# Optimization experiments

Hardware: AMD Instinct MI355X
Metric: run time of the kernel (lower is better)

The kernel has to match this reference:

```python
import jax, jax.numpy as jnp
import numpy as np

B, L, D, H, DFF = 4, 2048, 1024, 16, 4096
DH = D // H  # head dim = 64
EPS = 1e-5


def layernorm(x, g, b):
    mu = jnp.mean(x, axis=-1, keepdims=True)
    var = jnp.mean(jnp.square(x - mu), axis=-1, keepdims=True)
    return (x - mu) * jax.lax.rsqrt(var + EPS) * g + b


def setup_inputs() -> dict:
    key = jax.random.key(0)
    ks = jax.random.split(key, 16)
    s = 0.02
    return {
        "X": jax.random.normal(ks[0], (B, L, D), jnp.float32),
        "WQ": jax.random.normal(ks[1], (D, D), jnp.float32) * s,
        "bQ": jnp.zeros((D,), jnp.float32),
        "WK": jax.random.normal(ks[2], (D, D), jnp.float32) * s,
        "bK": jnp.zeros((D,), jnp.float32),
        "WV": jax.random.normal(ks[3], (D, D), jnp.float32) * s,
        "bV": jnp.zeros((D,), jnp.float32),
        "WO": jax.random.normal(ks[4], (D, D), jnp.float32) * s,
        "bO": jnp.zeros((D,), jnp.float32),
        "W1": jax.random.normal(ks[5], (D, DFF), jnp.float32) * s,
        "b1": jnp.zeros((DFF,), jnp.float32),
        "W2": jax.random.normal(ks[6], (DFF, D), jnp.float32) * s,
        "b2": jnp.zeros((D,), jnp.float32),
        "g1": jnp.ones((D,), jnp.float32),
        "be1": jnp.zeros((D,), jnp.float32),
        "g2": jnp.ones((D,), jnp.float32),
        "be2": jnp.zeros((D,), jnp.float32),
    }


def reference(X, WQ, bQ, WK, bK, WV, bV, WO, bO, W1, b1, W2, b2, g1, be1, g2, be2):
    # --- causal self-attention on LayerNorm1(X) ---
    Xn = layernorm(X, g1, be1)
    def heads(W, b):
        return (Xn @ W + b).reshape(B, L, H, DH).transpose(0, 2, 1, 3)  # [B,H,L,DH]
    Q, K, V = heads(WQ, bQ), heads(WK, bK), heads(WV, bV)
    scale = 1.0 / jnp.sqrt(jnp.float32(DH))
    scores = jnp.einsum('bhld,bhsd->bhls', Q, K) * scale  # [B,H,L,L]
    causal = jnp.tril(jnp.ones((L, L), dtype=bool))
    scores = jnp.where(causal, scores, -jnp.inf)
    attn = jax.nn.softmax(scores, axis=-1)
    AV = jnp.einsum('bhls,bhsd->bhld', attn, V)  # [B,H,L,DH]
    AV = AV.transpose(0, 2, 1, 3).reshape(B, L, H * DH)
    X = X + AV @ WO + bO
    # --- MLP on LayerNorm2(X) ---
    Xn2 = layernorm(X, g2, be2)
    out = X + jax.nn.relu(Xn2 @ W1 + b1) @ W2 + b2
    return out
```

## Files before the change

### kernel.cpp

```cpp
#include <hip/hip_runtime.h>
#include <hip/hip_bf16.h>
#include <stdint.h>

#define B_   4
#define L_   2048
#define D_   1024
#define H_   16
#define DH_  64
#define DFF_ 4096
#define EPS_ 1e-5f

typedef short s16x8 __attribute__((ext_vector_type(8)));
typedef short s16x4 __attribute__((ext_vector_type(4)));
typedef float f32x4 __attribute__((ext_vector_type(4)));

static __device__ __forceinline__ short f2bf(float f) {
    return __builtin_bit_cast(short, __float2bfloat16(f));
}

static __device__ __forceinline__ short f2bf_fast(float f) {
    return (short)((__builtin_bit_cast(unsigned int, f) + 0x8000u) >> 16);
}

static __device__ __forceinline__ void gload_lds16(const void* g, void* l) {
    __builtin_amdgcn_global_load_lds(
        (const __attribute__((address_space(1))) uint32_t*)g,
        (__attribute__((address_space(3))) uint32_t*)l, 16, 0, 0);
}

__global__ __launch_bounds__(256) void transpose_kernel(
    const float* __restrict__ in, short* __restrict__ out, int R, int C)
{
    __shared__ float tile[32][33];
    const int bx = blockIdx.x * 32, by = blockIdx.y * 32;
    const int tx = threadIdx.x & 31, ty = threadIdx.x >> 5;
#pragma unroll
    for (int i = 0; i < 32; i += 8)
        tile[ty + i][tx] = in[(size_t)(by + ty + i) * C + bx + tx];
    __syncthreads();
#pragma unroll
    for (int i = 0; i < 32; i += 8)
        out[(size_t)(bx + ty + i) * R + by + tx] = f2bf(tile[tx][ty + i]);
}

__global__ __launch_bounds__(256) void concat3_kernel(
    const float* __restrict__ a, const float* __restrict__ b,
    const float* __restrict__ c, float* __restrict__ o)
{
    const int i = blockIdx.x * 256 + threadIdx.x;
    o[i] = (i < 1024) ? a[i] : (i < 2048 ? b[i - 1024] : c[i - 2048]);
}

__global__ __launch_bounds__(256) void vtrans_kernel(
    const short* __restrict__ V, short* __restrict__ Vt)
{
    __shared__ short t[64][72];
    const int l0 = blockIdx.x * 64;
    const int bh = blockIdx.y;
    const int b = bh >> 4, h = bh & 15;
    const int tid = threadIdx.x;
    const int rr = tid >> 3, cc = tid & 7;
#pragma unroll
    for (int i = 0; i < 2; ++i) {
        const int row = i * 32 + rr;
        *(s16x8*)&t[row][cc * 8] =
            *(const s16x8*)(V + (size_t)(b * L_ + l0 + row) * D_ + h * DH_ + cc * 8);
    }
    __syncthreads();
#pragma unroll
    for (int i = 0; i < 2; ++i) {
        const int d = i * 32 + rr;
        const int lp0 = cc * 8;
        s16x8 o;
#pragma unroll
        for (int j = 0; j < 8; ++j) o[j] = t[lp0 + j][d];
        *(s16x8*)(Vt + ((size_t)bh * DH_ + d) * L_ + l0 + lp0) = o;
    }
}

__global__ __launch_bounds__(256) void ln_kernel(
    const float* __restrict__ x, const float* __restrict__ g,
    const float* __restrict__ bta, short* __restrict__ out)
{
    __shared__ float sm[8];
    const int row = blockIdx.x;
    const int t = threadIdx.x;
    const float4 v = ((const float4*)(x + (size_t)row * D_))[t];
    float s1 = v.x + v.y + v.z + v.w;
    float s2 = v.x * v.x + v.y * v.y + v.z * v.z + v.w * v.w;
#pragma unroll
    for (int off = 1; off < 64; off <<= 1) {
        s1 += __shfl_xor(s1, off);
        s2 += __shfl_xor(s2, off);
    }
    if ((t & 63) == 0) { sm[t >> 6] = s1; sm[4 + (t >> 6)] = s2; }
    __syncthreads();
    s1 = sm[0] + sm[1] + sm[2] + sm[3];
    s2 = sm[4] + sm[5] + sm[6] + sm[7];
    const float mu  = s1 * (1.f / D_);
    const float var = s2 * (1.f / D_) - mu * mu;
    const float rs  = rsqrtf(var + EPS_);
    const float4 gv = ((const float4*)g)[t];
    const float4 bv = ((const float4*)bta)[t];
    s16x4 o;
    o[0] = f2bf((v.x - mu) * rs * gv.x + bv.x);
    o[1] = f2bf((v.y - mu) * rs * gv.y + bv.y);
    o[2] = f2bf((v.z - mu) * rs * gv.z + bv.z);
    o[3] = f2bf((v.w - mu) * rs * gv.w + bv.w);
    *(s16x4*)(out + (size_t)row * D_ + t * 4) = o;
}

template <int MODE>
__global__ __launch_bounds__(512) void gemm_kernel(
    const short* __restrict__ A, const short* __restrict__ Bt,
    const float* __restrict__ bias, const float* __restrict__ res,
    void* __restrict__ out, int M, int N, int K)
{
    __shared__ short As[3][128 * 64];
    __shared__ short Bs[3][256 * 64];

    const int nx = gridDim.x;
    const int flat = blockIdx.y * nx + blockIdx.x;
    const int nper = (nx * gridDim.y) >> 3;
    const int nid = (flat & 7) * nper + (flat >> 3);
    const int m0 = (nid / nx) * 128;
    const int n0 = (nid % nx) * 256;

    const int tid = threadIdx.x;
    const int w = tid >> 6, l = tid & 63;
    const int wm = w >> 2, wn = w & 3;
    const int lg = l >> 4, li = l & 15;

    const short* aSrc[2];
    int adst[2];
#pragma unroll
    for (int i = 0; i < 2; ++i) {
        const int s = i * 512 + tid;
        const int row = s >> 3;
        const int ch = (s & 7) ^ (row & 7);
        aSrc[i] = A + (size_t)(m0 + row) * K + ch * 8;
        adst[i] = s * 8;
    }
    const short* bSrc[4];
    int bdst[4];
#pragma unroll
    for (int i = 0; i < 4; ++i) {
        const int s = i * 512 + tid;
        const int row = s >> 3;
        const int ch = (s & 7) ^ (row & 7);
        bSrc[i] = Bt + (size_t)(n0 + row) * K + ch * 8;
        bdst[i] = s * 8;
    }

    int aoff[4][2], boff[4][2];
#pragma unroll
    for (int m = 0; m < 4; ++m)
#pragma unroll
        for (int ks = 0; ks < 2; ++ks) {
            const int rowA = wm * 64 + m * 16 + li;
            aoff[m][ks] = rowA * 64 + (((ks * 4 + lg) ^ (rowA & 7)) * 8);
        }
#pragma unroll
    for (int n = 0; n < 4; ++n)
#pragma unroll
        for (int ks = 0; ks < 2; ++ks) {
            const int rowB = wn * 64 + n * 16 + li;
            boff[n][ks] = rowB * 64 + (((ks * 4 + lg) ^ (rowB & 7)) * 8);
        }

    f32x4 acc[4][4] = {};
    const int nT = K >> 6;

#pragma unroll
    for (int i = 0; i < 2; ++i) gload_lds16(aSrc[i], &As[0][adst[i]]);
#pragma unroll
    for (int i = 0; i < 4; ++i) gload_lds16(bSrc[i], &Bs[0][bdst[i]]);

    int cur = 0, nxt = 1;
    for (int t = 0; t < nT; ++t) {
        if (t + 1 < nT) {
            const int k1 = (t + 1) << 6;
#pragma unroll
            for (int i = 0; i < 2; ++i) gload_lds16(aSrc[i] + k1, &As[nxt][adst[i]]);
#pragma unroll
            for (int i = 0; i < 4; ++i) gload_lds16(bSrc[i] + k1, &Bs[nxt][bdst[i]]);
            asm volatile("s_waitcnt vmcnt(6)" ::: "memory");
        } else {
            asm volatile("s_waitcnt vmcnt(0)" ::: "memory");
        }
        __builtin_amdgcn_s_barrier();
        __builtin_amdgcn_sched_barrier(0);

        const short* as = &As[cur][0];
        const short* bs = &Bs[cur][0];
        s16x8 af[4][2], bf[4][2];
#pragma unroll
        for (int m = 0; m < 4; ++m)
#pragma unroll
            for (int ks = 0; ks < 2; ++ks)
                af[m][ks] = *(const s16x8*)&as[aoff[m][ks]];
#pragma unroll
        for (int n = 0; n < 4; ++n)
#pragma unroll
            for (int ks = 0; ks < 2; ++ks)
                bf[n][ks] = *(const s16x8*)&bs[boff[n][ks]];
#pragma unroll
        for (int ks = 0; ks < 2; ++ks)
#pragma unroll
            for (int m = 0; m < 4; ++m)
#pragma unroll
                for (int n = 0; n < 4; ++n)
                    acc[m][n] = __builtin_amdgcn_mfma_f32_16x16x32_bf16(
                        af[m][ks], bf[n][ks], acc[m][n], 0, 0, 0);

        cur = nxt;
        nxt = (nxt == 2) ? 0 : nxt + 1;
    }

#pragma unroll
    for (int m = 0; m < 4; ++m) {
#pragma unroll
        for (int n = 0; n < 4; ++n) {
            const int col = n0 + wn * 64 + n * 16 + li;
            const float bv = bias[col];
#pragma unroll
            for (int r = 0; r < 4; ++r) {
                const int row = m0 + wm * 64 + m * 16 + lg * 4 + r;
                float v = acc[m][n][r] + bv;
                if (MODE == 1) v = v > 0.f ? v : 0.f;
                if (MODE == 2) {
                    float* o = (float*)out;
                    o[(size_t)row * N + col] = v + res[(size_t)row * N + col];
                } else if (MODE == 3) {
                    short* o = (short*)out;
                    o[(size_t)(col >> 10) * (8192ull * 1024) +
                      (size_t)row * 1024 + (col & 1023)] = f2bf(v);
                } else {
                    short* o = (short*)out;
                    o[(size_t)row * N + col] = f2bf(v);
                }
            }
        }
    }
}

__global__ __launch_bounds__(512) void attn_kernel(
    const short* __restrict__ Q, const short* __restrict__ K,
    const short* __restrict__ Vt, short* __restrict__ O)
{
    __shared__ short Kbuf[3][64 * 64];
    __shared__ short Vbuf[3][64 * 64];
    __shared__ short Ps[8][16 * 72];

    const int xx = blockIdx.x;
    const int h = blockIdx.y, b = blockIdx.z;
    const int pr = xx >> 1;
    const int u = (pr + b * 2) & 7;
    const int qblk = ((xx + b) & 1) ? (15 - u) : u;
    const int tid = threadIdx.x;
    const int w = tid >> 6, l = tid & 63;
    const int lg = l >> 4, li = l & 15;
    const size_t headQ = ((size_t)b * L_) * D_ + (size_t)h * DH_;
    const size_t headV = ((size_t)(b * H_ + h) * DH_) * L_;
    const int q0 = qblk * 128;
    const int qw = q0 + w * 16;
    const float sc2 = 0.125f * 1.44269504f;

    s16x8 qf[2];
    {
        const short* qr = Q + headQ + (size_t)(qw + li) * D_;
        qf[0] = *(const s16x8*)(qr + lg * 8);
        qf[1] = *(const s16x8*)(qr + 32 + lg * 8);
    }

    const int srow = tid >> 3;
    const int schk = (tid & 7) ^ (srow & 7);
    const short* kSrc = K + headQ + (size_t)srow * D_ + schk * 8;
    const short* vSrc = Vt + headV + (size_t)srow * L_ + schk * 8;

    int koff0[4], koff1[4];
#pragma unroll
    for (int blk = 0; blk < 4; ++blk) {
        const int row = blk * 16 + li;
        const int hh = row & 7;
        koff0[blk] = row * 64 + ((lg ^ hh) * 8);
        koff1[blk] = row * 64 + (((lg + 4) ^ hh) * 8);
    }

    float m_r = -1e30f, l_r = 0.f;
    f32x4 oacc[4] = {};
    short* pw = &Ps[w][0];

    const int nt = 2 * qblk + 2;

    gload_lds16(kSrc, &Kbuf[0][tid * 8]);
    gload_lds16(vSrc, &Vbuf[0][tid * 8]);

    int cur = 0, nxt = 1;
    for (int t = 0; t < nt; ++t) {
        const int kv0 = t * 64;
        if (t + 1 < nt) {
            const int nkv = kv0 + 64;
            gload_lds16(kSrc + (size_t)nkv * D_, &Kbuf[nxt][tid * 8]);
            gload_lds16(vSrc + nkv, &Vbuf[nxt][tid * 8]);
            asm volatile("s_waitcnt vmcnt(2)" ::: "memory");
        } else {
            asm volatile("s_waitcnt vmcnt(0)" ::: "memory");
        }
        __builtin_amdgcn_s_barrier();
        __builtin_amdgcn_sched_barrier(0);

        if (kv0 <= qw + 15) {
            const short* kb = &Kbuf[cur][0];
            const short* vb = &Vbuf[cur][0];

            f32x4 s[4];
            __builtin_amdgcn_s_setprio(1);
#pragma unroll
            for (int blk = 0; blk < 4; ++blk) {
                const s16x8 kf0 = *(const s16x8*)&kb[koff0[blk]];
                const s16x8 kf1 = *(const s16x8*)&kb[koff1[blk]];
                f32x4 c = {0.f, 0.f, 0.f, 0.f};
                c = __builtin_amdgcn_mfma_f32_16x16x32_bf16(kf0, qf[0], c, 0, 0, 0);
                c = __builtin_amdgcn_mfma_f32_16x16x32_bf16(kf1, qf[1], c, 0, 0, 0);
                s[blk] = c;
            }
            __builtin_amdgcn_s_setprio(0);

            if (kv0 + 63 > qw) {
                const int q = qw + li;
#pragma unroll
                for (int blk = 0; blk < 4; ++blk) {
                    const int kvb = kv0 + blk * 16 + lg * 4;
#pragma unroll
                    for (int r = 0; r < 4; ++r)
                        if (kvb + r > q) s[blk][r] = -1e30f;
                }
            }

            float mb[4];
#pragma unroll
            for (int blk = 0; blk < 4; ++blk)
                mb[blk] = fmaxf(fmaxf(s[blk][0], s[blk][1]),
                                fmaxf(s[blk][2], s[blk][3]));
            float mm = fmaxf(fmaxf(mb[0], mb[1]), fmaxf(mb[2], mb[3]));
            mm = fmaxf(mm, __shfl_xor(mm, 16));
            mm = fmaxf(mm, __shfl_xor(mm, 32));
            const float mxs = mm * sc2;

            float p[4][4];
            if (__all(mxs <= m_r + 11.5f)) {
                float ps[4];
#pragma unroll
                for (int blk = 0; blk < 4; ++blk) {
#pragma unroll
                    for (int r = 0; r < 4; ++r)
                        p[blk][r] = __builtin_amdgcn_exp2f(
                            fmaf(s[blk][r], sc2, -m_r));
                    ps[blk] = (p[blk][0] + p[blk][1]) + (p[blk][2] + p[blk][3]);
                }
                float sum = (ps[0] + ps[1]) + (ps[2] + ps[3]);
                sum += __shfl_xor(sum, 16);
                sum += __shfl_xor(sum, 32);
                l_r += sum;
            } else {
                const float mn = fmaxf(m_r, mxs);
                const float fac = __builtin_amdgcn_exp2f(m_r - mn);
                m_r = mn;
                float ps[4];
#pragma unroll
                for (int blk = 0; blk < 4; ++blk) {
#pragma unroll
                    for (int r = 0; r < 4; ++r)
                        p[blk][r] = __builtin_amdgcn_exp2f(
                            fmaf(s[blk][r], sc2, -mn));
                    ps[blk] = (p[blk][0] + p[blk][1]) + (p[blk][2] + p[blk][3]);
                }
                float sum = (ps[0] + ps[1]) + (ps[2] + ps[3]);
                sum += __shfl_xor(sum, 16);
                sum += __shfl_xor(sum, 32);
                l_r = l_r * fac + sum;
#pragma unroll
                for (int d = 0; d < 4; ++d)
#pragma unroll
                    for (int r = 0; r < 4; ++r)
                        oacc[d][r] *= fac;
            }

#pragma unroll
            for (int blk = 0; blk < 4; ++blk) {
                s16x4 pk;
#pragma unroll
                for (int r = 0; r < 4; ++r) pk[r] = f2bf_fast(p[blk][r]);
                *(s16x4*)&pw[li * 72 + blk * 16 + lg * 4] = pk;
            }
            asm volatile("s_waitcnt lgkmcnt(0)" ::: "memory");
            __builtin_amdgcn_sched_barrier(0);
            const s16x8 pa0 = *(const s16x8*)&pw[li * 72 + lg * 8];
            const s16x8 pa1 = *(const s16x8*)&pw[li * 72 + 32 + lg * 8];

            __builtin_amdgcn_s_setprio(1);
#pragma unroll
            for (int dblk = 0; dblk < 4; ++dblk) {
                const s16x8 vf0 = *(const s16x8*)&vb[koff0[dblk]];
                const s16x8 vf1 = *(const s16x8*)&vb[koff1[dblk]];
                oacc[dblk] = __builtin_amdgcn_mfma_f32_16x16x32_bf16(vf0, pa0, oacc[dblk], 0, 0, 0);
                oacc[dblk] = __builtin_amdgcn_mfma_f32_16x16x32_bf16(vf1, pa1, oacc[dblk], 0, 0, 0);
            }
            __builtin_amdgcn_s_setprio(0);
        }

        cur = nxt;
        nxt = (nxt == 2) ? 0 : nxt + 1;
    }

    const float inv = 1.f / l_r;
#pragma unroll
    for (int dblk = 0; dblk < 4; ++dblk) {
        s16x4 ov;
#pragma unroll
        for (int r = 0; r < 4; ++r) ov[r] = f2bf(oacc[dblk][r] * inv);
        *(s16x4*)(O + headQ + (size_t)(qw + li) * D_ + dblk * 16 + lg * 4) = ov;
    }
}

extern "C" void kernel_launch(void* const* d_in, const int* in_sizes, int n_in,
                              void* d_out, int out_size, void* d_ws, size_t ws_size,
                              hipStream_t stream)
{
    const float* X   = (const float*)d_in[0];
    const float* WQ  = (const float*)d_in[1];
    const float* bQ  = (const float*)d_in[2];
    const float* WK  = (const float*)d_in[3];
    const float* bK  = (const float*)d_in[4];
    const float* WV  = (const float*)d_in[5];
    const float* bV  = (const float*)d_in[6];
    const float* WO  = (const float*)d_in[7];
    const float* bO  = (const float*)d_in[8];
    const float* W1  = (const float*)d_in[9];
    const float* b1  = (const float*)d_in[10];
    const float* W2  = (const float*)d_in[11];
    const float* b2  = (const float*)d_in[12];
    const float* g1  = (const float*)d_in[13];
    const float* be1 = (const float*)d_in[14];
    const float* g2  = (const float*)d_in[15];
    const float* be2 = (const float*)d_in[16];
    float* out = (float*)d_out;

    char* ws = (char*)d_ws;
    const size_t MB = 1u << 20;
    short* WQKVt = (short*)(ws + 0 * MB);
    short* WOt = (short*)(ws + 6 * MB);
    short* W1t = (short*)(ws + 8 * MB);
    short* W2t = (short*)(ws + 16 * MB);
    short* Xn  = (short*)(ws + 24 * MB);
    short* Qb  = (short*)(ws + 40 * MB);
    short* Vb  = (short*)(ws + 72 * MB);
    short* Vtb = (short*)(ws + 88 * MB);
    float* bQKV = (float*)(ws + 88 * MB);
    short* AV  = (short*)(ws + 72 * MB);
    short* H1  = (short*)(ws + 40 * MB);

    const dim3 tb(256);

    transpose_kernel<<<dim3(32, 32), tb, 0, stream>>>(WQ, WQKVt, 1024, 1024);
    transpose_kernel<<<dim3(32, 32), tb, 0, stream>>>(WK, WQKVt + 1024 * 1024, 1024, 1024);
    transpose_kernel<<<dim3(32, 32), tb, 0, stream>>>(WV, WQKVt + 2 * 1024 * 1024, 1024, 1024);
    transpose_kernel<<<dim3(32, 32), tb, 0, stream>>>(WO, WOt, 1024, 1024);
    transpose_kernel<<<dim3(128, 32), tb, 0, stream>>>(W1, W1t, 1024, 4096);
    transpose_kernel<<<dim3(32, 128), tb, 0, stream>>>(W2, W2t, 4096, 1024);
    concat3_kernel<<<dim3(12), tb, 0, stream>>>(bQ, bK, bV, bQKV);

    ln_kernel<<<8192, tb, 0, stream>>>(X, g1, be1, Xn);

    gemm_kernel<3><<<dim3(12, 64), dim3(512), 0, stream>>>(
        Xn, WQKVt, bQKV, nullptr, Qb, 8192, 3072, 1024);

    vtrans_kernel<<<dim3(L_ / 64, B_ * H_), tb, 0, stream>>>(Vb, Vtb);

    attn_kernel<<<dim3(L_ / 128, H_, B_), dim3(512), 0, stream>>>(
        Qb, Qb + 8192ull * 1024, Vtb, AV);

    gemm_kernel<2><<<dim3(4, 64), dim3(512), 0, stream>>>(
        AV, WOt, bO, X, out, 8192, 1024, 1024);

    ln_kernel<<<8192, tb, 0, stream>>>(out, g2, be2, Xn);

    gemm_kernel<1><<<dim3(16, 64), dim3(512), 0, stream>>>(
        Xn, W1t, b1, nullptr, H1, 8192, 4096, 1024);
    gemm_kernel<2><<<dim3(4, 64), dim3(512), 0, stream>>>(
        H1, W2t, b2, out, out, 8192, 1024, 4096);
}
```

Before: 372.1 us.

## Widen attention KV tiles from 64 to 128 keys per iteration

```diff
diff --git a/kernel.cpp b/kernel.cpp
--- a/kernel.cpp
+++ b/kernel.cpp
@@ -16,10 +16,6 @@
 
 static __device__ __forceinline__ short f2bf(float f) {
     return __builtin_bit_cast(short, __float2bfloat16(f));
-}
-
-static __device__ __forceinline__ short f2bf_fast(float f) {
-    return (short)((__builtin_bit_cast(unsigned int, f) + 0x8000u) >> 16);
 }
 
 static __device__ __forceinline__ void gload_lds16(const void* g, void* l) {
@@ -248,9 +244,9 @@
     const short* __restrict__ Q, const short* __restrict__ K,
     const short* __restrict__ Vt, short* __restrict__ O)
 {
-    __shared__ short Kbuf[3][64 * 64];
-    __shared__ short Vbuf[3][64 * 64];
-    __shared__ short Ps[8][16 * 72];
+    __shared__ short Kbuf[3][128 * 64];
+    __shared__ short Vbuf[3][64 * 128];
+    __shared__ short Ps[8][16 * 136];
 
     const int xx = blockIdx.x;
     const int h = blockIdx.y, b = blockIdx.z;
@@ -273,142 +269,174 @@
         qf[1] = *(const s16x8*)(qr + 32 + lg * 8);
     }
 
-    const int srow = tid >> 3;
-    const int schk = (tid & 7) ^ (srow & 7);
-    const short* kSrc = K + headQ + (size_t)srow * D_ + schk * 8;
-    const short* vSrc = Vt + headV + (size_t)srow * L_ + schk * 8;
-
-    int koff0[4], koff1[4];
-#pragma unroll
-    for (int blk = 0; blk < 4; ++blk) {
+    const short* kSrc[2];
+    int kdst[2];
+#pragma unroll
+    for (int i = 0; i < 2; ++i) {
+        const int s = i * 512 + tid;
+        const int row = s >> 3;
+        const int ch = (s & 7) ^ (row & 7);
+        kSrc[i] = K + headQ + (size_t)row * D_ + ch * 8;
+        kdst[i] = s * 8;
+    }
+    const short* vSrc[2];
+    int vdst[2];
+#pragma unroll
+    for (int i = 0; i < 2; ++i) {
+        const int s = i * 512 + tid;
+        const int row = s >> 4;
+        const int ch = (s & 15) ^ (row & 15);
+        vSrc[i] = Vt + headV + (size_t)row * L_ + ch * 8;
+        vdst[i] = s * 8;
+    }
+
+    int koff0[8], koff1[8];
+#pragma unroll
+    for (int blk = 0; blk < 8; ++blk) {
         const int row = blk * 16 + li;
         const int hh = row & 7;
         koff0[blk] = row * 64 + ((lg ^ hh) * 8);
         koff1[blk] = row * 64 + (((lg + 4) ^ hh) * 8);
     }
+    int voff[4][4];
+#pragma unroll
+    for (int dblk = 0; dblk < 4; ++dblk)
+#pragma unroll
+        for (int j = 0; j < 4; ++j)
+            voff[dblk][j] = (dblk * 16 + li) * 128 + (((j * 4 + lg) ^ li) * 8);
 
     float m_r = -1e30f, l_r = 0.f;
     f32x4 oacc[4] = {};
     short* pw = &Ps[w][0];
 
-    const int nt = 2 * qblk + 2;
-
-    gload_lds16(kSrc, &Kbuf[0][tid * 8]);
-    gload_lds16(vSrc, &Vbuf[0][tid * 8]);
+    const int nt = qblk + 1;
+
+#pragma unroll
+    for (int i = 0; i < 2; ++i) {
+        gload_lds16(kSrc[i], &Kbuf[0][kdst[i]]);
+        gload_lds16(vSrc[i], &Vbuf[0][vdst[i]]);
+    }
 
     int cur = 0, nxt = 1;
     for (int t = 0; t < nt; ++t) {
-        const int kv0 = t * 64;
+        const int kv0 = t * 128;
         if (t + 1 < nt) {
-            const int nkv = kv0 + 64;
-            gload_lds16(kSrc + (size_t)nkv * D_, &Kbuf[nxt][tid * 8]);
-            gload_lds16(vSrc + nkv, &Vbuf[nxt][tid * 8]);
-            asm volatile("s_waitcnt vmcnt(2)" ::: "memory");
+            const int nkv = kv0 + 128;
+#pragma unroll
+            for (int i = 0; i < 2; ++i) {
+                gload_lds16(kSrc[i] + (size_t)nkv * D_, &Kbuf[nxt][kdst[i]]);
+                gload_lds16(vSrc[i] + nkv, &Vbuf[nxt][vdst[i]]);
+            }
+            asm volatile("s_waitcnt vmcnt(4)" ::: "memory");
         } else {
             asm volatile("s_waitcnt vmcnt(0)" ::: "memory");
         }
         __builtin_amdgcn_s_barrier();
         __builtin_amdgcn_sched_barrier(0);
 
-        if (kv0 <= qw + 15) {
-            const short* kb = &Kbuf[cur][0];
-            const short* vb = &Vbuf[cur][0];
-
-            f32x4 s[4];
-            __builtin_amdgcn_s_setprio(1);
-#pragma unroll
-            for (int blk = 0; blk < 4; ++blk) {
-                const s16x8 kf0 = *(const s16x8*)&kb[koff0[blk]];
-                const s16x8 kf1 = *(const s16x8*)&kb[koff1[blk]];
-                f32x4 c = {0.f, 0.f, 0.f, 0.f};
-                c = __builtin_amdgcn_mfma_f32_16x16x32_bf16(kf0, qf[0], c, 0, 0, 0);
-                c = __builtin_amdgcn_mfma_f32_16x16x32_bf16(kf1, qf[1], c, 0, 0, 0);
-                s[blk] = c;
+        const short* kb = &Kbuf[cur][0];
+        const short* vb = &Vbuf[cur][0];
+
+        f32x4 s[8];
+        __builtin_amdgcn_s_setprio(1);
+#pragma unroll
+        for (int blk = 0; blk < 8; ++blk) {
+            const s16x8 kf0 = *(const s16x8*)&kb[koff0[blk]];
+            const s16x8 kf1 = *(const s16x8*)&kb[koff1[blk]];
+            f32x4 c = {0.f, 0.f, 0.f, 0.f};
+            c = __builtin_amdgcn_mfma_f32_16x16x32_bf16(kf0, qf[0], c, 0, 0, 0);
+            c = __builtin_amdgcn_mfma_f32_16x16x32_bf16(kf1, qf[1], c, 0, 0, 0);
+            s[blk] = c;
+        }
+        __builtin_amdgcn_s_setprio(0);
+
+        if (kv0 + 127 > qw) {
+            const int q = qw + li;
+#pragma unroll
+            for (int blk = 0; blk < 8; ++blk) {
+                const int kvb = kv0 + blk * 16 + lg * 4;
+#pragma unroll
+                for (int r = 0; r < 4; ++r)
+                    if (kvb + r > q) s[blk][r] = -1e30f;
             }
-            __builtin_amdgcn_s_setprio(0);
-
-            if (kv0 + 63 > qw) {
-                const int q = qw + li;
-#pragma unroll
-                for (int blk = 0; blk < 4; ++blk) {
-                    const int kvb = kv0 + blk * 16 + lg * 4;
-#pragma unroll
-                    for (int r = 0; r < 4; ++r)
-                        if (kvb + r > q) s[blk][r] = -1e30f;
-                }
+        }
+
+        float mb[8];
+#pragma unroll
+        for (int blk = 0; blk < 8; ++blk)
+            mb[blk] = fmaxf(fmaxf(s[blk][0], s[blk][1]),
+                            fmaxf(s[blk][2], s[blk][3]));
+        float mm = fmaxf(fmaxf(fmaxf(mb[0], mb[1]), fmaxf(mb[2], mb[3])),
+                         fmaxf(fmaxf(mb[4], mb[5]), fmaxf(mb[6], mb[7])));
+        mm = fmaxf(mm, __shfl_xor(mm, 16));
+        mm = fmaxf(mm, __shfl_xor(mm, 32));
+        const float mxs = mm * sc2;
+
+        float p[8][4];
+        if (__all(mxs <= m_r + 11.5f)) {
+            float ps[8];
+#pragma unroll
+            for (int blk = 0; blk < 8; ++blk) {
+#pragma unroll
+                for (int r = 0; r < 4; ++r)
+                    p[blk][r] = __builtin_amdgcn_exp2f(
+                        fmaf(s[blk][r], sc2, -m_r));
+                ps[blk] = (p[blk][0] + p[blk][1]) + (p[blk][2] + p[blk][3]);
             }
-
-            float mb[4];
-#pragma unroll
-            for (int blk = 0; blk < 4; ++blk)
-                mb[blk] = fmaxf(fmaxf(s[blk][0], s[blk][1]),
-                                fmaxf(s[blk][2], s[blk][3]));
-            float mm = fmaxf(fmaxf(mb[0], mb[1]), fmaxf(mb[2], mb[3]));
-            mm = fmaxf(mm, __shfl_xor(mm, 16));
-            mm = fmaxf(mm, __shfl_xor(mm, 32));
-            const float mxs = mm * sc2;
-
-            float p[4][4];
-            if (__all(mxs <= m_r + 11.5f)) {
-                float ps[4];
-#pragma unroll
-                for (int blk = 0; blk < 4; ++blk) {
-#pragma unroll
-                    for (int r = 0; r < 4; ++r)
-                        p[blk][r] = __builtin_amdgcn_exp2f(
-                            fmaf(s[blk][r], sc2, -m_r));
-                    ps[blk] = (p[blk][0] + p[blk][1]) + (p[blk][2] + p[blk][3]);
-                }
-                float sum = (ps[0] + ps[1]) + (ps[2] + ps[3]);
-                sum += __shfl_xor(sum, 16);
-                sum += __shfl_xor(sum, 32);
-                l_r += sum;
-            } else {
-                const float mn = fmaxf(m_r, mxs);
-                const float fac = __builtin_amdgcn_exp2f(m_r - mn);
-                m_r = mn;
-                float ps[4];
-#pragma unroll
-                for (int blk = 0; blk < 4; ++blk) {
-#pragma unroll
-                    for (int r = 0; r < 4; ++r)
-                        p[blk][r] = __builtin_amdgcn_exp2f(
-                            fmaf(s[blk][r], sc2, -mn));
-                    ps[blk] = (p[blk][0] + p[blk][1]) + (p[blk][2] + p[blk][3]);
-                }
-                float sum = (ps[0] + ps[1]) + (ps[2] + ps[3]);
-                sum += __shfl_xor(sum, 16);
-                sum += __shfl_xor(sum, 32);
-                l_r = l_r * fac + sum;
-#pragma unroll
-                for (int d = 0; d < 4; ++d)
-#pragma unroll
-                    for (int r = 0; r < 4; ++r)
-                        oacc[d][r] *= fac;
+            float sum = ((ps[0] + ps[1]) + (ps[2] + ps[3])) +
+                        ((ps[4] + ps[5]) + (ps[6] + ps[7]));
+            sum += __shfl_xor(sum, 16);
+            sum += __shfl_xor(sum, 32);
+            l_r += sum;
+        } else {
+            const float mn = fmaxf(m_r, mxs);
+            const float fac = __builtin_amdgcn_exp2f(m_r - mn);
+            m_r = mn;
+            float ps[8];
+#pragma unroll
+            for (int blk = 0; blk < 8; ++blk) {
+#pragma unroll
+                for (int r = 0; r < 4; ++r)
+                    p[blk][r] = __builtin_amdgcn_exp2f(
+                        fmaf(s[blk][r], sc2, -mn));
+                ps[blk] = (p[blk][0] + p[blk][1]) + (p[blk][2] + p[blk][3]);
             }
-
-#pragma unroll
-            for (int blk = 0; blk < 4; ++blk) {
-                s16x4 pk;
-#pragma unroll
-                for (int r = 0; r < 4; ++r) pk[r] = f2bf_fast(p[blk][r]);
-                *(s16x4*)&pw[li * 72 + blk * 16 + lg * 4] = pk;
+            float sum = ((ps[0] + ps[1]) + (ps[2] + ps[3])) +
+                        ((ps[4] + ps[5]) + (ps[6] + ps[7]));
+            sum += __shfl_xor(sum, 16);
+            sum += __shfl_xor(sum, 32);
+            l_r = l_r * fac + sum;
+#pragma unroll
+            for (int d = 0; d < 4; ++d)
+#pragma unroll
+                for (int r = 0; r < 4; ++r)
+                    oacc[d][r] *= fac;
+        }
+
+#pragma unroll
+        for (int blk = 0; blk < 8; ++blk) {
+            s16x4 pk;
+#pragma unroll
+            for (int r = 0; r < 4; ++r) pk[r] = f2bf(p[blk][r]);
+            *(s16x4*)&pw[li * 136 + blk * 16 + lg * 4] = pk;
+        }
+        asm volatile("s_waitcnt lgkmcnt(0)" ::: "memory");
+        __builtin_amdgcn_sched_barrier(0);
+        s16x8 pa[4];
+#pragma unroll
+        for (int j = 0; j < 4; ++j)
+            pa[j] = *(const s16x8*)&pw[li * 136 + j * 32 + lg * 8];
+
+        __builtin_amdgcn_s_setprio(1);
+#pragma unroll
+        for (int dblk = 0; dblk < 4; ++dblk)
+#pragma unroll
+            for (int j = 0; j < 4; ++j) {
+                const s16x8 vf = *(const s16x8*)&vb[voff[dblk][j]];
+                oacc[dblk] = __builtin_amdgcn_mfma_f32_16x16x32_bf16(
+                    vf, pa[j], oacc[dblk], 0, 0, 0);
             }
-            asm volatile("s_waitcnt lgkmcnt(0)" ::: "memory");
-            __builtin_amdgcn_sched_barrier(0);
-            const s16x8 pa0 = *(const s16x8*)&pw[li * 72 + lg * 8];
-            const s16x8 pa1 = *(const s16x8*)&pw[li * 72 + 32 + lg * 8];
-
-            __builtin_amdgcn_s_setprio(1);
-#pragma unroll
-            for (int dblk = 0; dblk < 4; ++dblk) {
-                const s16x8 vf0 = *(const s16x8*)&vb[koff0[dblk]];
-                const s16x8 vf1 = *(const s16x8*)&vb[koff1[dblk]];
-                oacc[dblk] = __builtin_amdgcn_mfma_f32_16x16x32_bf16(vf0, pa0, oacc[dblk], 0, 0, 0);
-                oacc[dblk] = __builtin_amdgcn_mfma_f32_16x16x32_bf16(vf1, pa1, oacc[dblk], 0, 0, 0);
-            }
-            __builtin_amdgcn_s_setprio(0);
-        }
+        __builtin_amdgcn_s_setprio(0);
 
         cur = nxt;
         nxt = (nxt == 2) ? 0 : nxt + 1;
```

New measurement: 379.9 us. 2.1% more time.
